# Kernel tuning notes

Measured on AMD Instinct MI355X. Metric: run time of the kernel, lower is better.

The kernel has to match this reference:

```python
import jax, jax.numpy as jnp
import numpy as np
from jax import lax

V, E, H, B, LP, LQ = 50000, 300, 150, 32, 400, 50


def setup_inputs() -> dict:
    key = jax.random.key(0)
    ks = iter(jax.random.split(key, 40))

    def nrm(shape, s=0.05):
        return jax.random.normal(next(ks), shape, jnp.float32) * s

    emb = nrm((V, E)).at[0].set(0.0)  # padding_idx=0 row is zero
    return dict(
        passage_ids=jax.random.randint(next(ks), (LP, B), 1, V, jnp.int32),
        question_ids=jax.random.randint(next(ks), (LQ, B), 1, V, jnp.int32),
        passage_lens=jax.random.randint(next(ks), (B,), LP // 2, LP + 1, jnp.int32),
        question_lens=jax.random.randint(next(ks), (B,), LQ // 2, LQ + 1, jnp.int32),
        emb=emb,
        plstm_Wih=nrm((4 * H, E)), plstm_Whh=nrm((4 * H, H)), plstm_b=nrm((4 * H,)),
        Wq=nrm((H, H)), Wp=nrm((H, H)), bp=nrm((H,)), Wr=nrm((H, H)),
        wa=nrm((H,)), ba=nrm(()),
        mf_Wih=nrm((4 * H, 2 * H)), mf_Whh=nrm((4 * H, H)), mf_b=nrm((4 * H,)),
        mb_Wih=nrm((4 * H, 2 * H)), mb_Whh=nrm((4 * H, H)), mb_b=nrm((4 * H,)),
        Vm=nrm((H, 2 * H)), Wa_ans=nrm((H, H)), ba_ans=nrm((H,)),
        wb=nrm((H,)), bb=nrm(()),
        ap_Wih=nrm((4 * H, 2 * H)), ap_Whh=nrm((4 * H, H)), ap_b=nrm((4 * H,)),
    )


def _cell(x, h, c, Wih, Whh, b):
    # torch LSTMCell: gate order i, f, g, o; b = b_ih + b_hh
    g = x @ Wih.T + h @ Whh.T + b
    i, f, gg, o = jnp.split(g, 4, axis=-1)
    c2 = jax.nn.sigmoid(f) * c + jax.nn.sigmoid(i) * jnp.tanh(gg)
    return jax.nn.sigmoid(o) * jnp.tanh(c2), c2


def _run_lstm(x, Wih, Whh, b):
    z = jnp.zeros((x.shape[1], Whh.shape[1]), x.dtype)

    def step(carry, xt):
        h, c = carry
        h2, c2 = _cell(xt, h, c, Wih, Whh, b)
        return (h2, c2), h2

    return lax.scan(step, (z, z), x)[1]


def reference(passage_ids, question_ids, passage_lens, question_lens, emb,
              plstm_Wih, plstm_Whh, plstm_b, Wq, Wp, bp, Wr, wa, ba,
              mf_Wih, mf_Whh, mf_b, mb_Wih, mb_Whh, mb_b,
              Vm, Wa_ans, ba_ans, wb, bb, ap_Wih, ap_Whh, ap_b):
    p_mask = (jnp.arange(LP)[:, None] < passage_lens[None, :]).astype(jnp.float32)  # [LP,B]
    q_mask = (jnp.arange(LQ)[:, None] < question_lens[None, :]).astype(jnp.float32)  # [LQ,B]
    # NB: original code (bug) encodes BOTH passage and question with passage_lstm
    Hp = _run_lstm(emb[passage_ids], plstm_Wih, plstm_Whh, plstm_b) * p_mask[:, :, None]
    Hq = _run_lstm(emb[question_ids], plstm_Wih, plstm_Whh, plstm_b) * q_mask[:, :, None]
    aq = Hq @ Wq.T  # [LQ,B,H]

    def match(Hp_seq, m_seq, Wih, Whh, b):
        z0 = jnp.zeros((B, H), jnp.float32)

        def step(carry, inputs):
            h, c = carry
            hp_t, m_t = inputs  # [B,H], [B]
            g = jnp.tanh(aq + (hp_t @ Wp.T + bp)[None] + (h @ Wr.T)[None])  # [LQ,B,H]
            alpha = jax.nn.softmax(g @ wa + ba, axis=0)  # softmax over question positions, [LQ,B]
            wq_t = jnp.einsum('lb,lbh->bh', alpha, Hq)
            zt = jnp.concatenate([hp_t, wq_t], axis=-1) * m_t[:, None]
            h2, c2 = _cell(zt, h, c, Wih, Whh, b)
            h2 = h2 * m_t[:, None]
            c2 = c2 * m_t[:, None]
            return (h2, c2), h2

        return lax.scan(step, (z0, z0), (Hp_seq, m_seq))[1]

    Hf = match(Hp, p_mask, mf_Wih, mf_Whh, mf_b)                    # [LP,B,H]
    Hb = match(Hp[::-1], p_mask[::-1], mb_Wih, mb_Whh, mb_b)[::-1]  # [LP,B,H]
    Hr = jnp.concatenate([Hf, Hb], axis=-1)  # [LP,B,2H]
    am = Hr @ Vm.T  # [LP,B,H]

    ha = jnp.zeros((B, H), jnp.float32)
    ca = jnp.zeros((B, H), jnp.float32)
    dists = []
    for _ in range(2):  # answer-pointer: start / end
        Fk = jnp.tanh(am + (ha @ Wa_ans.T + ba_ans)[None])
        beta = jax.nn.softmax(Fk @ wb + bb, axis=0)  # [LP,B]
        dists.append(beta)
        wHr = jnp.einsum('lb,lbh->bh', beta, Hr)
        ha, ca = _cell(wHr, ha, ca, ap_Wih, ap_Whh, ap_b)
    return jnp.stack(dists)  # [2, LP, B]
```

## Files before the change

### kernel.cpp

```cpp
#include <hip/hip_runtime.h>


typedef _Float16 f16;
typedef f16 f16x2 __attribute__((ext_vector_type(2)));
typedef unsigned int u32;
typedef unsigned short u16;

constexpr int cLP = 400, cLQ = 50, cB = 32, cH = 150, cG = 600;

__device__ __forceinline__ float exp2_(float x){
#if __has_builtin(__builtin_amdgcn_exp2f)
  return __builtin_amdgcn_exp2f(x);
#else
  return exp2f(x);
#endif
}
__device__ __forceinline__ float rcp_(float x){
#if __has_builtin(__builtin_amdgcn_rcpf)
  return __builtin_amdgcn_rcpf(x);
#else
  return 1.0f / x;
#endif
}
__device__ __forceinline__ float sigm(float x){ return rcp_(1.f + exp2_(-1.44269504f * x)); }
__device__ __forceinline__ float tanh_(float x){ return 1.f - 2.f * rcp_(1.f + exp2_(2.88539008f * x)); }

union U2 { u32 u; f16x2 h; };

__device__ __forceinline__ float fdot2_(u32 a, u32 b, float c){
  U2 ua, ub; ua.u = a; ub.u = b;
#if __has_builtin(__builtin_amdgcn_fdot2)
  return __builtin_amdgcn_fdot2(ua.h, ub.h, c, false);
#else
  return c + (float)ua.h[0] * (float)ub.h[0] + (float)ua.h[1] * (float)ub.h[1];
#endif
}
__device__ __forceinline__ u32 pack2(float x, float y){
  U2 p; p.h[0] = (f16)x; p.h[1] = (f16)y; return p.u;
}
__device__ __forceinline__ float2 unp2(u32 v){
  U2 p; p.u = v; return make_float2((float)p.h[0], (float)p.h[1]);
}

__device__ __forceinline__ uint4 ldw4(const float* __restrict__ wr, int i){
  uint4 r;
  r.x = pack2(wr[8*i+0], wr[8*i+1]);
  r.y = pack2(wr[8*i+2], wr[8*i+3]);
  r.z = pack2(wr[8*i+4], wr[8*i+5]);
  r.w = pack2(wr[8*i+6], wr[8*i+7]);
  return r;
}

#define PIN4(v) asm volatile("" : "+v"(v.x), "+v"(v.y), "+v"(v.z), "+v"(v.w));
#define PIN4W(i) PIN4(w##i)
#define PIN4Q(i) PIN4(q##i)

#define REP10(M) M(0) M(1) M(2) M(3) M(4) M(5) M(6) M(7) M(8) M(9)
#define REP6(M) M(0) M(1) M(2) M(3) M(4) M(5)

__global__ __launch_bounds__(256)
void gemm_k(const float* __restrict__ A, const int* __restrict__ ids,
            const float* __restrict__ emb,
            const float* __restrict__ W, int ldw, const float* __restrict__ bias,
            float* __restrict__ Cf, f16* __restrict__ Ch,
            int M, int N, int K)
{
  __shared__ __align__(16) float As[16][68];
  __shared__ __align__(16) float Wt[16][68];
  __shared__ int sids[64];
  int tid = threadIdx.x;
  int n0 = blockIdx.x * 64;
  int m0 = blockIdx.y * 64;
  int tx = tid & 15, ty = tid >> 4;
  if (ids){ if (tid < 64) sids[tid] = ids[m0 + tid]; }
  __syncthreads();

  float acc[4][4] = {};
  int sm = tid >> 2;
  int kq = (tid & 3) << 2;
  const float* arow = ids ? (emb + (size_t)sids[sm] * K)
                          : (A   + (size_t)(m0 + sm) * K);
  const float* wrow = W + (size_t)(n0 + sm) * ldw;
  bool nok = (n0 + sm) < N;

  for (int k0 = 0; k0 < K; k0 += 16){
    #pragma unroll
    for (int p = 0; p < 4; p++){
      int kk = kq + p, k = k0 + kk;
      As[kk][sm] = (k < K) ? arow[k] : 0.f;
      Wt[kk][sm] = (nok && k < K) ? wrow[k] : 0.f;
    }
    __syncthreads();
    #pragma unroll
    for (int kk = 0; kk < 16; kk++){
      float4 av = *(const float4*)&As[kk][ty << 2];
      float4 wv = *(const float4*)&Wt[kk][tx << 2];
      float a[4] = {av.x, av.y, av.z, av.w};
      float w[4] = {wv.x, wv.y, wv.z, wv.w};
      #pragma unroll
      for (int i = 0; i < 4; i++)
        #pragma unroll
        for (int j = 0; j < 4; j++)
          acc[i][j] += a[i] * w[j];
    }
    __syncthreads();
  }
  float bj[4];
  #pragma unroll
  for (int j = 0; j < 4; j++){
    int n = n0 + (tx << 2) + j;
    bj[j] = (bias && n < N) ? bias[n] : 0.f;
  }
  #pragma unroll
  for (int i = 0; i < 4; i++){
    int m = m0 + (ty << 2) + i;
    #pragma unroll
    for (int j = 0; j < 4; j++){
      int n = n0 + (tx << 2) + j;
      if (n < N){
        size_t ci = (size_t)m * N + n;
        float v = acc[i][j] + bj[j];
        if (Ch) Ch[ci] = (f16)v; else Cf[ci] = v;
      }
    }
  }
}

__attribute__((amdgpu_waves_per_eu(1, 3)))
__global__ __launch_bounds__(640)
void enc_k(const float* __restrict__ XGp, const float* __restrict__ XGq,
           const float* __restrict__ Whh,
           const int* __restrict__ plens, const int* __restrict__ qlens,
           float* __restrict__ Hp, float* __restrict__ Hq)
{
  int wg = blockIdx.x;
  bool isq = wg >= cB;
  int b = wg & (cB - 1);
  const float* XG = isq ? XGq : XGp;
  float* Hout = isq ? Hq : Hp;
  int T   = isq ? cLQ : cLP;
  int len = (isq ? qlens : plens)[b];
  int tid = threadIdx.x;

  __shared__ __align__(16) u32 WhhL4[9 * 600 * 4];
  __shared__ float c[cH], gl[cG];
  __shared__ __align__(16) u32 h2s[80];

#define DECLW(i) uint4 w##i;
  REP10(DECLW)
#undef DECLW
  {
    const float* wr = Whh + (size_t)(tid < cG ? tid : 0) * cH;
#define LOADW(i) w##i = ldw4(wr, i);
    REP10(LOADW)
#undef LOADW
    REP10(PIN4W)
  }
  for (int idx = tid; idx < 9 * 600; idx += 640){
    int p4 = idx / 600, r = idx % 600;
    const float* wrow = Whh + (size_t)r * cH + 80;
    uint4 v;
    if (p4 < 8) v = ldw4(wrow, p4);
    else {
      v.x = pack2(wrow[64], wrow[65]);
      v.y = pack2(wrow[66], wrow[67]);
      v.z = pack2(wrow[68], wrow[69]);
      v.w = 0;
    }
    *(uint4*)&WhhL4[idx * 4] = v;
  }
  if (tid < cH) c[tid] = 0.f;
  if (tid < 80) h2s[tid] = 0;
  __syncthreads();

  float xgCur = 0.f;
  if (tid < cG) xgCur = XG[(size_t)b * cG + tid];

  for (int t = 0; t < T; t++){
    int tn = (t + 1 < T) ? t + 1 : t;
    float xgN = 0.f;
    if (tid < cG) xgN = XG[((size_t)tn * cB + b) * cG + tid];

    if (tid < cG){
      float aA = 0.f, aB = 0.f, aC = 0.f, aD = 0.f;
#define DOTW(i) { uint4 hq = *(const uint4*)&h2s[4*(i)]; \
      aA = fdot2_(hq.x, w##i.x, aA); aB = fdot2_(hq.y, w##i.y, aB); \
      aC = fdot2_(hq.z, w##i.z, aC); aD = fdot2_(hq.w, w##i.w, aD); }
      REP10(DOTW)
#undef DOTW
      #pragma unroll
      for (int p4 = 0; p4 < 9; p4++){
        uint4 hq = *(const uint4*)&h2s[40 + 4 * p4];
        uint4 wv = *(const uint4*)&WhhL4[(p4 * 600 + tid) * 4];
        aA = fdot2_(hq.x, wv.x, aA);
        aB = fdot2_(hq.y, wv.y, aB);
        aC = fdot2_(hq.z, wv.z, aC);
        aD = fdot2_(hq.w, wv.w, aD);
      }
      gl[tid] = xgCur + ((aA + aB) + (aC + aD));
    }
    __syncthreads();
    if (tid < 75){
      float hv[2];
      #pragma unroll
      for (int z = 0; z < 2; z++){
        int u = 2 * tid + z;
        float ig = sigm(gl[u]);
        float fg = sigm(gl[cH + u]);
        float gg = tanh_(gl[2 * cH + u]);
        float og = sigm(gl[3 * cH + u]);
        float c2 = fg * c[u] + ig * gg;
        float hh = og * tanh_(c2);
        c[u] = c2;
        hv[z] = hh;
      }
      h2s[tid] = pack2(hv[0], hv[1]);
      float mk = (t < len) ? 1.f : 0.f;
      float2 st; st.x = hv[0] * mk; st.y = hv[1] * mk;
      *(float2*)&Hout[((size_t)t * cB + b) * cH + 2 * tid] = st;
    }
    __syncthreads();
    xgCur = xgN;
  }
}

__attribute__((amdgpu_waves_per_eu(1, 3)))
__global__ __launch_bounds__(640)
void match_k(const f16* __restrict__ XAf, const f16* __restrict__ XAb,
             const f16* __restrict__ QWf, const f16* __restrict__ QWb,
             const float* __restrict__ aq, const float* __restrict__ pp,
             const float* __restrict__ mfWhh, const float* __restrict__ mbWhh,
             const float* __restrict__ mfb, const float* __restrict__ mbb,
             const float* __restrict__ Wr, const float* __restrict__ wa,
             const int* __restrict__ plens, float* __restrict__ Hr)
{
  constexpr int NPAD = 160;
  int wg = blockIdx.x;
  int dir = wg >> 5;
  int b = wg & 31;
  const f16* XA = dir ? XAb : XAf;
  const f16* QW = dir ? QWb : QWf;
  const float* Whh = dir ? mbWhh : mfWhh;
  const float* bm  = dir ? mbb   : mfb;
  int len = plens[b];
  int tid = threadIdx.x;

  __shared__ __align__(16) u32 WhhL4[9 * 600 * 4];
  __shared__ __align__(16) u32 WrT4[19 * 150 * 4];
  __shared__ __align__(16) u32 aq3[cLQ * 96];
  __shared__ float gl[cG];
  __shared__ __align__(16) float sc[NPAD];
  __shared__ __align__(16) float waS[NPAD];
  __shared__ float c[cH];
  __shared__ __align__(16) u32 h2s[80];
  __shared__ float loge[64];
  __shared__ __align__(16) u32 alpha2[28];

#define DECLW(i) uint4 w##i;
  REP10(DECLW)
#undef DECLW
  float bk = 0.f;
  {
    const float* wr = Whh + (size_t)(tid < cG ? tid : 0) * cH;
#define LOADW(i) w##i = ldw4(wr, i);
    REP10(LOADW)
#undef LOADW
    REP10(PIN4W)
    if (tid < cG) bk = bm[tid];
  }
#define DECLQ(i) uint4 q##i;
  REP6(DECLQ)
#undef DECLQ
  u32 q24s;
  {
    const u16* QWu = (const u16*)QW;
    int row = (tid < cG) ? tid : 0;
#define QP(p) ((u32)QWu[((size_t)(2*(p)) * cB + b) * cG + row] | \
               ((u32)QWu[((size_t)(2*(p)+1) * cB + b) * cG + row] << 16))
#define LOADQ(i) q##i.x = QP(4*(i)+0); q##i.y = QP(4*(i)+1); \
                 q##i.z = QP(4*(i)+2); q##i.w = QP(4*(i)+3);
    LOADQ(0) LOADQ(1) LOADQ(2) LOADQ(3) LOADQ(4) LOADQ(5)
    q24s = QP(24);
#undef LOADQ
#undef QP
    REP6(PIN4Q)
    asm volatile("" : "+v"(q24s));
  }
  for (int idx = tid; idx < 9 * 600; idx += 640){
    int p4 = idx / 600, r = idx % 600;
    const float* wrow = Whh + (size_t)r * cH + 80;
    uint4 v;
    if (p4 < 8) v = ldw4(wrow, p4);
    else {
      v.x = pack2(wrow[64], wrow[65]);
      v.y = pack2(wrow[66], wrow[67]);
      v.z = pack2(wrow[68], wrow[69]);
      v.w = 0;
    }
    *(uint4*)&WhhL4[idx * 4] = v;
  }
  for (int idx = tid; idx < 19 * 150; idx += 640){
    int i = idx / 150, j = idx % 150;
    const float* wrow = Wr + (size_t)j * cH;
    uint4 v;
    if (i < 18) v = ldw4(wrow, i);
    else {
      v.x = pack2(wrow[144], wrow[145]);
      v.y = pack2(wrow[146], wrow[147]);
      v.z = pack2(wrow[148], wrow[149]);
      v.w = 0;
    }
    *(uint4*)&WrT4[idx * 4] = v;
  }
  for (int idx = tid; idx < cLQ * 96; idx += 640){
    int l = idx / 96, s = idx % 96;
    int ch = s / 12, t = s % 12;
    u32 v = 0;
    if (t < 10){
      int p = ch * 10 + t;
      if (p < 75){
        const float* ap = aq + ((size_t)l * cB + b) * cH;
        v = pack2(ap[2 * p], ap[2 * p + 1]);
      }
    }
    aq3[idx] = v;
  }
  for (int i = tid; i < NPAD; i += 640) waS[i] = (i < cH) ? wa[i] : 0.f;
  if (tid < cH) c[tid] = 0.f;
  if (tid < 80) h2s[tid] = 0;
  if (tid >= cH && tid < NPAD) sc[tid] = 0.f;
  if (tid >= 25 && tid < 28) alpha2[tid] = 0;
  __syncthreads();

  f16 xaCurH = (f16)0.f, xaNxtH = (f16)0.f;
  float ppCur = 0.f, ppNxt = 0.f;
  {
    int t0 = dir ? (cLP - 1) : 0;
    if (tid < cG) xaCurH = XA[((size_t)t0 * cB + b) * cG + tid];
    if (tid < cH) ppCur = pp[((size_t)t0 * cB + b) * cH + tid];
  }

  for (int s = 0; s < cLP; s++){
    int tt = dir ? (cLP - 1 - s) : s;
    float mk = (tt < len) ? 1.f : 0.f;

    {
      int sn = (s + 1 < cLP) ? s + 1 : s;
      int tn = dir ? (cLP - 1 - sn) : sn;
      if (tid < cG) xaNxtH = XA[((size_t)tn * cB + b) * cG + tid];
      if (tid < cH) ppNxt = pp[((size_t)tn * cB + b) * cH + tid];
    }

    if (tid < cH){
      float sA = 0.f, sB = 0.f, sC = 0.f, sD = 0.f;
      #pragma unroll
      for (int i = 0; i < 19; i++){
        uint4 hq = *(const uint4*)&h2s[4 * i];
        uint4 wv = *(const uint4*)&WrT4[(i * 150 + tid) * 4];
        sA = fdot2_(hq.x, wv.x, sA);
        sB = fdot2_(hq.y, wv.y, sB);
        sC = fdot2_(hq.z, wv.z, sC);
        sD = fdot2_(hq.w, wv.w, sD);
      }
      sc[tid] = ((sA + sB) + (sC + sD)) + ppCur;
    }
    __syncthreads();

    if (tid < 400){
      int l = tid >> 3, q = tid & 7;
      const u32* ab = aq3 + l * 96 + q * 12;
      uint4 A0 = *(const uint4*)(ab);
      uint4 A1 = *(const uint4*)(ab + 4);
      uint2 A2 = *(const uint2*)(ab + 8);
      u32 aqp[10] = {A0.x, A0.y, A0.z, A0.w, A1.x, A1.y, A1.z, A1.w, A2.x, A2.y};
      const float4* scv = (const float4*)(sc  + 20 * q);
      const float4* wav = (const float4*)(waS + 20 * q);
      float p0 = 0.f, p1 = 0.f;
      #pragma unroll
      for (int i = 0; i < 5; i++){
        float4 sv = scv[i];
        float4 wv = wav[i];
        float2 a0 = unp2(aqp[2 * i]);
        float2 a1 = unp2(aqp[2 * i + 1]);
        p0 += wv.x * rcp_(1.f + exp2_(2.88539008f * (a0.x + sv.x)));
        p1 += wv.y * rcp_(1.f + exp2_(2.88539008f * (a0.y + sv.y)));
        p0 += wv.z * rcp_(1.f + exp2_(2.88539008f * (a1.x + sv.z)));
        p1 += wv.w * rcp_(1.f + exp2_(2.88539008f * (a1.y + sv.w)));
      }
      float part = p0 + p1;
      part += __shfl_xor(part, 1);
      part += __shfl_xor(part, 2);
      part += __shfl_xor(part, 4);
      if (q == 0) loge[l] = part;
    }
    __syncthreads();

    if (tid < 64){
      float lg = (tid < cLQ) ? (-2.f * loge[tid]) : -1e30f;
      float mx = lg;
      #pragma unroll
      for (int off = 32; off; off >>= 1) mx = fmaxf(mx, __shfl_xor(mx, off));
      float e = (tid < cLQ) ? exp2_((lg - mx) * 1.44269504f) : 0.f;
      float sum = e;
      #pragma unroll
      for (int off = 32; off; off >>= 1) sum += __shfl_xor(sum, off);
      float al = e * rcp_(sum);
      float alhi = __shfl_down(al, 1);
      if (tid < cLQ && !(tid & 1)) alpha2[tid >> 1] = pack2(al, alhi);
    }
    __syncthreads();

    if (tid < cG){
      float aA = 0.f, aB = 0.f, aC = 0.f, aD = 0.f;
#define DOTW(i) { uint4 hq = *(const uint4*)&h2s[4*(i)]; \
      aA = fdot2_(hq.x, w##i.x, aA); aB = fdot2_(hq.y, w##i.y, aB); \
      aC = fdot2_(hq.z, w##i.z, aC); aD = fdot2_(hq.w, w##i.w, aD); }
      REP10(DOTW)
#undef DOTW
      #pragma unroll
      for (int p4 = 0; p4 < 9; p4++){
        uint4 hq = *(const uint4*)&h2s[40 + 4 * p4];
        uint4 wv = *(const uint4*)&WhhL4[(p4 * 600 + tid) * 4];
        aA = fdot2_(hq.x, wv.x, aA);
        aB = fdot2_(hq.y, wv.y, aB);
        aC = fdot2_(hq.z, wv.z, aC);
        aD = fdot2_(hq.w, wv.w, aD);
      }
      float qA = 0.f, qB = 0.f;
#define DOTQ(i) { uint4 a4 = *(const uint4*)&alpha2[4*(i)]; \
      qA = fdot2_(a4.x, q##i.x, qA); qB = fdot2_(a4.y, q##i.y, qB); \
      qA = fdot2_(a4.z, q##i.z, qA); qB = fdot2_(a4.w, q##i.w, qB); }
      REP6(DOTQ)
#undef DOTQ
      qA = fdot2_(alpha2[24], q24s, qA);
      float acc = ((aA + aB) + (aC + aD));
      gl[tid] = bk + acc + mk * ((float)xaCurH + (qA + qB));
    }
    __syncthreads();

    if (tid < 75){
      float hv[2];
      #pragma unroll
      for (int z = 0; z < 2; z++){
        int u = 2 * tid + z;
        float ig = sigm(gl[u]);
        float fg = sigm(gl[cH + u]);
        float gg = tanh_(gl[2 * cH + u]);
        float og = sigm(gl[3 * cH + u]);
        float c2 = (fg * c[u] + ig * gg) * mk;
        float hh = og * tanh_(c2) * mk;
        c[u] = c2;
        hv[z] = hh;
      }
      h2s[tid] = pack2(hv[0], hv[1]);
      float2 st; st.x = hv[0]; st.y = hv[1];
      *(float2*)&Hr[((size_t)tt * cB + b) * (2 * cH) + dir * cH + 2 * tid] = st;
    }
    __syncthreads();

    xaCurH = xaNxtH;
    ppCur  = ppNxt;
  }
}

__global__ __launch_bounds__(640)
void ptr_k(const float* __restrict__ am, const float* __restrict__ Hr,
           const float* __restrict__ Wa, const float* __restrict__ baa,
           const float* __restrict__ wb,
           const float* __restrict__ apWih, const float* __restrict__ apWhh,
             const float* __restrict__ apb, float* __restrict__ out)
{
  int b = blockIdx.x, tid = threadIdx.x;
  __shared__ float ha[cH], ca[cH], haWa[160], wbs[160];
  __shared__ float beta[cLP], wHr[2 * cH], gl[cG], red[20];
  if (tid < cH){ ha[tid] = 0.f; ca[tid] = 0.f; }
  if (tid < 160) wbs[tid] = (tid < cH) ? wb[tid] : 0.f;
  __syncthreads();

  for (int it = 0; it < 2; ++it){
    if (tid < cH){
      float acc = baa[tid];
      const float* wr = Wa + (size_t)tid * cH;
      for (int i = 0; i < cH; i++) acc += ha[i] * wr[i];
      haWa[tid] = acc;
    } else if (tid < 160) haWa[tid] = 0.f;
    __syncthreads();

    {
      int tt = tid >> 4;
      int jq = tid & 15;
      for (int t0 = 0; t0 < cLP; t0 += 40){
        int t = t0 + tt;
        float part = 0.f;
        const float* amr = am + ((size_t)t * cB + b) * cH;
        #pragma unroll
        for (int i = 0; i < 10; i++){
          int j = jq * 10 + i;
          if (j < cH){
            float F = tanh_(amr[j] + haWa[j]);
            part += wbs[j] * F;
          }
        }
        part += __shfl_xor(part, 1);
        part += __shfl_xor(part, 2);
        part += __shfl_xor(part, 4);
        part += __shfl_xor(part, 8);
        if (jq == 0) beta[t] = part;
      }
    }
    __syncthreads();

    float x = (tid < cLP) ? beta[tid] : -1e30f;
    float mx = x;
    #pragma unroll
    for (int off = 32; off; off >>= 1) mx = fmaxf(mx, __shfl_xor(mx, off));
    if ((tid & 63) == 0) red[tid >> 6] = mx;
    __syncthreads();
    if (tid == 0){
      float m2 = red[0];
      for (int w = 1; w < 10; w++) m2 = fmaxf(m2, red[w]);
      red[16] = m2;
    }
    __syncthreads();
    mx = red[16];
    float e = (tid < cLP) ? exp2_((x - mx) * 1.44269504f) : 0.f;
    float sm = e;
    #pragma unroll
    for (int off = 32; off; off >>= 1) sm += __shfl_xor(sm, off);
    if ((tid & 63) == 0) red[tid >> 6] = sm;
    __syncthreads();
    if (tid == 0){
      float s2 = 0.f;
      for (int w = 0; w < 10; w++) s2 += red[w];
      red[17] = s2;
    }
    __syncthreads();
    float bsum = red[17];
    if (tid < cLP){
      float bt = e * rcp_(bsum);
      beta[tid] = bt;
      out[(size_t)it * cLP * cB + (size_t)tid * cB + b] = bt;
    }
    __syncthreads();

    if (tid < 2 * cH){
      float acc = 0.f;
      for (int t = 0; t < cLP; t++)
        acc += beta[t] * Hr[((size_t)t * cB + b) * (2 * cH) + tid];
      wHr[tid] = acc;
    }
    __syncthreads();

    if (tid < cG){
      float acc = apb[tid];
      const float* r1 = apWih + (size_t)tid * (2 * cH);
      for (int i = 0; i < 2 * cH; i++) acc += wHr[i] * r1[i];
      const float* r2 = apWhh + (size_t)tid * cH;
      for (int i = 0; i < cH; i++) acc += ha[i] * r2[i];
      gl[tid] = acc;
    }
    __syncthreads();
    if (tid < cH){
      float ig = sigm(gl[tid]);
      float fg = sigm(gl[cH + tid]);
      float gg = tanh_(gl[2 * cH + tid]);
      float og = sigm(gl[3 * cH + tid]);
      float c2 = fg * ca[tid] + ig * gg;
      ca[tid] = c2;
      ha[tid] = og * tanh_(c2);
    }
    __syncthreads();
  }
}

extern "C" void kernel_launch(void* const* d_in, const int* in_sizes, int n_in,
                              void* d_out, int out_size, void* d_ws, size_t ws_size,
                              hipStream_t stream)
{
  (void)in_sizes; (void)n_in; (void)out_size; (void)ws_size;
  const int*   p_ids = (const int*)d_in[0];
  const int*   q_ids = (const int*)d_in[1];
  const int*   plens = (const int*)d_in[2];
  const int*   qlens = (const int*)d_in[3];
  const float* emb   = (const float*)d_in[4];
  const float* pWih  = (const float*)d_in[5];
  const float* pWhh  = (const float*)d_in[6];
  const float* pb    = (const float*)d_in[7];
  const float* Wq    = (const float*)d_in[8];
  const float* Wp    = (const float*)d_in[9];
  const float* bp    = (const float*)d_in[10];
  const float* Wr    = (const float*)d_in[11];
  const float* wa    = (const float*)d_in[12];
  const float* mfWih = (const float*)d_in[14];
  const float* mfWhh = (const float*)d_in[15];
  const float* mfb   = (const float*)d_in[16];
  const float* mbWih = (const float*)d_in[17];
  const float* mbWhh = (const float*)d_in[18];
  const float* mbb   = (const float*)d_in[19];
  const float* Vm    = (const float*)d_in[20];
  const float* Waa   = (const float*)d_in[21];
  const float* baa   = (const float*)d_in[22];
  const float* wb    = (const float*)d_in[23];
  const float* apWih = (const float*)d_in[25];
  const float* apWhh = (const float*)d_in[26];
  const float* apb   = (const float*)d_in[27];
  float* out = (float*)d_out;

  float* ws  = (float*)d_ws;
  float* XGp = ws;
  float* XGq = ws + 7680000;
  f16*   XAb = (f16*)(ws + 8640000);
  float* Hp  = ws + 12480000;
  float* Hq  = ws + 14400000;
  float* aqb = ws + 14640000;
  float* ppb = ws + 14880000;
  float* Hr  = ws + 16800000;
  float* am  = ws + 20640000;
  f16*   XAf = (f16*)XGp;
  f16*   QWf = (f16*)XGq;
  f16*   QWb = QWf + (size_t)1600 * 600;

  dim3 blk(256);
  gemm_k<<<dim3(10,200), blk, 0, stream>>>(nullptr, p_ids, emb, pWih, 300, pb,
                                           XGp, nullptr, 12800, 600, 300);
  gemm_k<<<dim3(10, 25), blk, 0, stream>>>(nullptr, q_ids, emb, pWih, 300, pb,
                                           XGq, nullptr, 1600, 600, 300);
  enc_k<<<64, 640, 0, stream>>>(XGp, XGq, pWhh, plens, qlens, Hp, Hq);
  gemm_k<<<dim3(3,200), blk, 0, stream>>>(Hp, nullptr, nullptr, Wp, 150, bp,
                                          ppb, nullptr, 12800, 150, 150);
  gemm_k<<<dim3(3, 25), blk, 0, stream>>>(Hq, nullptr, nullptr, Wq, 150, nullptr,
                                          aqb, nullptr, 1600, 150, 150);
  gemm_k<<<dim3(10,200), blk, 0, stream>>>(Hp, nullptr, nullptr, mfWih, 300, nullptr,
                                           nullptr, XAf, 12800, 600, 150);
  gemm_k<<<dim3(10,200), blk, 0, stream>>>(Hp, nullptr, nullptr, mbWih, 300, nullptr,
                                           nullptr, XAb, 12800, 600, 150);
  gemm_k<<<dim3(10, 25), blk, 0, stream>>>(Hq, nullptr, nullptr, mfWih + 150, 300, nullptr,
                                           nullptr, QWf, 1600, 600, 150);
  gemm_k<<<dim3(10, 25), blk, 0, stream>>>(Hq, nullptr, nullptr, mbWih + 150, 300, nullptr,
                                           nullptr, QWb, 1600, 600, 150);
  match_k<<<64, 640, 0, stream>>>(XAf, XAb, QWf, QWb, aqb, ppb, mfWhh, mbWhh,
                                  mfb, mbb, Wr, wa, plens, Hr);
  gemm_k<<<dim3(3,200), blk, 0, stream>>>(Hr, nullptr, nullptr, Vm, 300, nullptr,
                                          am, nullptr, 12800, 150, 300);
  ptr_k<<<32, 640, 0, stream>>>(am, Hr, Waa, baa, wb, apWih, apWhh, apb, out);
}
```

Before: 2.308 ms.

## Split Wr matvec across lanes and overlap Whh matvec with attention phase

The Wr·h matvec now uses all 600 threads, with four lanes per output summing partial dot products through shuffles instead of 150 threads each doing a full dot product. The recurrent Whh·h matvec no longer depends on alpha, so it moves before the attention-score stage and runs alongside it; the later stage only adds the alpha-weighted question term into gl. The LSTM cell update is spread over 150 threads (one unit each) rather than 75 threads handling two units, and h is stored as an f16 array. Together these aim to shorten the serial per-timestep critical path of the recurrence, at the cost of extra shuffles and a read-modify-write of gl.

```diff
diff --git a/kernel.cpp b/kernel.cpp
--- a/kernel.cpp
+++ b/kernel.cpp
@@ -246,13 +246,13 @@
   int tid = threadIdx.x;
 
   __shared__ __align__(16) u32 WhhL4[9 * 600 * 4];
-  __shared__ __align__(16) u32 WrT4[19 * 150 * 4];
+  __shared__ __align__(16) u32 WrT4[20 * 150 * 4];
   __shared__ __align__(16) u32 aq3[cLQ * 96];
   __shared__ float gl[cG];
   __shared__ __align__(16) float sc[NPAD];
   __shared__ __align__(16) float waS[NPAD];
   __shared__ float c[cH];
-  __shared__ __align__(16) u32 h2s[80];
+  __shared__ __align__(16) f16 hsf[160];
   __shared__ float loge[64];
   __shared__ __align__(16) u32 alpha2[28];
 
@@ -299,12 +299,12 @@
     }
     *(uint4*)&WhhL4[idx * 4] = v;
   }
-  for (int idx = tid; idx < 19 * 150; idx += 640){
+  for (int idx = tid; idx < 20 * 150; idx += 640){
     int i = idx / 150, j = idx % 150;
     const float* wrow = Wr + (size_t)j * cH;
-    uint4 v;
+    uint4 v = {0, 0, 0, 0};
     if (i < 18) v = ldw4(wrow, i);
-    else {
+    else if (i == 18){
       v.x = pack2(wrow[144], wrow[145]);
       v.y = pack2(wrow[146], wrow[147]);
       v.z = pack2(wrow[148], wrow[149]);
@@ -327,7 +327,7 @@
   }
   for (int i = tid; i < NPAD; i += 640) waS[i] = (i < cH) ? wa[i] : 0.f;
   if (tid < cH) c[tid] = 0.f;
-  if (tid < 80) h2s[tid] = 0;
+  if (tid < 160) hsf[tid] = (f16)0.f;
   if (tid >= cH && tid < NPAD) sc[tid] = 0.f;
   if (tid >= 25 && tid < 28) alpha2[tid] = 0;
   __syncthreads();
@@ -337,7 +337,8 @@
   {
     int t0 = dir ? (cLP - 1) : 0;
     if (tid < cG) xaCurH = XA[((size_t)t0 * cB + b) * cG + tid];
-    if (tid < cH) ppCur = pp[((size_t)t0 * cB + b) * cH + tid];
+    if (tid < cG && (tid & 3) == 0)
+      ppCur = pp[((size_t)t0 * cB + b) * cH + (tid >> 2)];
   }
 
   for (int s = 0; s < cLP; s++){
@@ -348,33 +349,57 @@
       int sn = (s + 1 < cLP) ? s + 1 : s;
       int tn = dir ? (cLP - 1 - sn) : sn;
       if (tid < cG) xaNxtH = XA[((size_t)tn * cB + b) * cG + tid];
-      if (tid < cH) ppNxt = pp[((size_t)tn * cB + b) * cH + tid];
-    }
-
-    if (tid < cH){
+      if (tid < cG && (tid & 3) == 0)
+        ppNxt = pp[((size_t)tn * cB + b) * cH + (tid >> 2)];
+    }
+
+    if (tid < cG){
+      int q = tid & 3, j = tid >> 2;
       float sA = 0.f, sB = 0.f, sC = 0.f, sD = 0.f;
       #pragma unroll
-      for (int i = 0; i < 19; i++){
-        uint4 hq = *(const uint4*)&h2s[4 * i];
-        uint4 wv = *(const uint4*)&WrT4[(i * 150 + tid) * 4];
+      for (int i0 = 0; i0 < 5; i0++){
+        int i = 5 * q + i0;
+        uint4 hq = *(const uint4*)&hsf[8 * i];
+        uint4 wv = *(const uint4*)&WrT4[(i * 150 + j) * 4];
         sA = fdot2_(hq.x, wv.x, sA);
         sB = fdot2_(hq.y, wv.y, sB);
         sC = fdot2_(hq.z, wv.z, sC);
         sD = fdot2_(hq.w, wv.w, sD);
       }
-      sc[tid] = ((sA + sB) + (sC + sD)) + ppCur;
-    }
-    __syncthreads();
-
+      float v = (sA + sB) + (sC + sD);
+      v += __shfl_xor(v, 1);
+      v += __shfl_xor(v, 2);
+      if (q == 0) sc[j] = v + ppCur;
+    }
+    __syncthreads();
+
+    if (tid < cG){
+      float aA = 0.f, aB = 0.f, aC = 0.f, aD = 0.f;
+#define DOTW(i) { uint4 hq = *(const uint4*)&hsf[8*(i)]; \
+      aA = fdot2_(hq.x, w##i.x, aA); aB = fdot2_(hq.y, w##i.y, aB); \
+      aC = fdot2_(hq.z, w##i.z, aC); aD = fdot2_(hq.w, w##i.w, aD); }
+      REP10(DOTW)
+#undef DOTW
+      #pragma unroll
+      for (int p4 = 0; p4 < 9; p4++){
+        uint4 hq = *(const uint4*)&hsf[80 + 8 * p4];
+        uint4 wv = *(const uint4*)&WhhL4[(p4 * 600 + tid) * 4];
+        aA = fdot2_(hq.x, wv.x, aA);
+        aB = fdot2_(hq.y, wv.y, aB);
+        aC = fdot2_(hq.z, wv.z, aC);
+        aD = fdot2_(hq.w, wv.w, aD);
+      }
+      gl[tid] = bk + ((aA + aB) + (aC + aD));
+    }
     if (tid < 400){
-      int l = tid >> 3, q = tid & 7;
-      const u32* ab = aq3 + l * 96 + q * 12;
+      int l = tid >> 3, q8 = tid & 7;
+      const u32* ab = aq3 + l * 96 + q8 * 12;
       uint4 A0 = *(const uint4*)(ab);
       uint4 A1 = *(const uint4*)(ab + 4);
       uint2 A2 = *(const uint2*)(ab + 8);
       u32 aqp[10] = {A0.x, A0.y, A0.z, A0.w, A1.x, A1.y, A1.z, A1.w, A2.x, A2.y};
-      const float4* scv = (const float4*)(sc  + 20 * q);
-      const float4* wav = (const float4*)(waS + 20 * q);
+      const float4* scv = (const float4*)(sc  + 20 * q8);
+      const float4* wav = (const float4*)(waS + 20 * q8);
       float p0 = 0.f, p1 = 0.f;
       #pragma unroll
       for (int i = 0; i < 5; i++){
@@ -391,7 +416,7 @@
       part += __shfl_xor(part, 1);
       part += __shfl_xor(part, 2);
       part += __shfl_xor(part, 4);
-      if (q == 0) loge[l] = part;
+      if (q8 == 0) loge[l] = part;
     }
     __syncthreads();
 
@@ -411,21 +436,6 @@
     __syncthreads();
 
     if (tid < cG){
-      float aA = 0.f, aB = 0.f, aC = 0.f, aD = 0.f;
-#define DOTW(i) { uint4 hq = *(const uint4*)&h2s[4*(i)]; \
-      aA = fdot2_(hq.x, w##i.x, aA); aB = fdot2_(hq.y, w##i.y, aB); \
-      aC = fdot2_(hq.z, w##i.z, aC); aD = fdot2_(hq.w, w##i.w, aD); }
-      REP10(DOTW)
-#undef DOTW
-      #pragma unroll
-      for (int p4 = 0; p4 < 9; p4++){
-        uint4 hq = *(const uint4*)&h2s[40 + 4 * p4];
-        uint4 wv = *(const uint4*)&WhhL4[(p4 * 600 + tid) * 4];
-        aA = fdot2_(hq.x, wv.x, aA);
-        aB = fdot2_(hq.y, wv.y, aB);
-        aC = fdot2_(hq.z, wv.z, aC);
-        aD = fdot2_(hq.w, wv.w, aD);
-      }
       float qA = 0.f, qB = 0.f;
 #define DOTQ(i) { uint4 a4 = *(const uint4*)&alpha2[4*(i)]; \
       qA = fdot2_(a4.x, q##i.x, qA); qB = fdot2_(a4.y, q##i.y, qB); \
@@ -433,28 +443,20 @@
       REP6(DOTQ)
 #undef DOTQ
       qA = fdot2_(alpha2[24], q24s, qA);
-      float acc = ((aA + aB) + (aC + aD));
-      gl[tid] = bk + acc + mk * ((float)xaCurH + (qA + qB));
-    }
-    __syncthreads();
-
-    if (tid < 75){
-      float hv[2];
-      #pragma unroll
-      for (int z = 0; z < 2; z++){
-        int u = 2 * tid + z;
-        float ig = sigm(gl[u]);
-        float fg = sigm(gl[cH + u]);
-        float gg = tanh_(gl[2 * cH + u]);
-        float og = sigm(gl[3 * cH + u]);
-        float c2 = (fg * c[u] + ig * gg) * mk;
-        float hh = og * tanh_(c2) * mk;
-        c[u] = c2;
-        hv[z] = hh;
-      }
-      h2s[tid] = pack2(hv[0], hv[1]);
-      float2 st; st.x = hv[0]; st.y = hv[1];
-      *(float2*)&Hr[((size_t)tt * cB + b) * (2 * cH) + dir * cH + 2 * tid] = st;
+      gl[tid] = gl[tid] + mk * ((float)xaCurH + (qA + qB));
+    }
+    __syncthreads();
+
+    if (tid < cH){
+      float ig = sigm(gl[tid]);
+      float fg = sigm(gl[cH + tid]);
+      float gg = tanh_(gl[2 * cH + tid]);
+      float og = sigm(gl[3 * cH + tid]);
+      float c2 = (fg * c[tid] + ig * gg) * mk;
+      float hh = og * tanh_(c2) * mk;
+      c[tid] = c2;
+      hsf[tid] = (f16)hh;
+      Hr[((size_t)tt * cB + b) * (2 * cH) + dir * cH + tid] = hh;
     }
     __syncthreads();
 
```

Result: faster. 2.238 ms (-3.0%).
